# Optimization experiments

Hardware: AMD Instinct MI355X
Metric: run time of the kernel (lower is better)

Reference implementation:

```python
import jax, jax.numpy as jnp
import numpy as np

B, P, H, W, K = 2, 4096, 128, 128, 8
RADIUS = 0.05  # NDC-space point radius (raster_settings.radius)


def setup_inputs() -> dict:
    key = jax.random.key(0)
    k1, k2, k3 = jax.random.split(key, 3)
    points_world = jax.random.normal(k1, (B, P, 3), jnp.float32)
    # near-identity rotation (row-vector convention: X_view = X_world @ R + T)
    R = jnp.eye(3, dtype=jnp.float32)[None] + 0.01 * jax.random.normal(k2, (B, 3, 3), jnp.float32)
    # translate cloud to z ~ +3 so points are in front of the camera
    T = (0.1 * jax.random.normal(k3, (B, 3), jnp.float32)).at[:, 2].add(3.0)
    focal = jnp.full((B,), 1.5, jnp.float32)
    return {"points_world": points_world, "R": R, "T": T, "focal": focal}


def reference(points_world, R, T, focal):
    # --- camera transform: world -> view -> NDC (z kept in view space) ---
    pts_view = jnp.einsum('bpi,bij->bpj', points_world, R) + T[:, None, :]  # [B,P,3]
    z = pts_view[..., 2]                                                    # [B,P]
    x_ndc = focal[:, None] * pts_view[..., 0] / z
    y_ndc = focal[:, None] * pts_view[..., 1] / z

    # --- pixel-center NDC grid (pytorch3d convention: +x left, +y up) ---
    gx = 1.0 - 2.0 * (jnp.arange(W, dtype=jnp.float32) + 0.5) / W  # [W]
    gy = 1.0 - 2.0 * (jnp.arange(H, dtype=jnp.float32) + 0.5) / H  # [H]
    GY, GX = jnp.meshgrid(gy, gx, indexing='ij')
    gxf = GX.reshape(-1)  # [HW]
    gyf = GY.reshape(-1)

    # --- per-pixel candidate search: squared NDC distance to every point ---
    dist2 = (gxf[None, :, None] - x_ndc[:, None, :]) ** 2 \
          + (gyf[None, :, None] - y_ndc[:, None, :]) ** 2      # [B,HW,P]
    inside = (dist2 < RADIUS * RADIUS) & (z[:, None, :] > 0.0)  # in radius & in front

    # --- depth-sorted top-K nearest-in-z among covering points ---
    keyz = jnp.where(inside, z[:, None, :], jnp.inf)            # [B,HW,P]
    neg_top, idx_top = jax.lax.top_k(-keyz, K)                  # K smallest z
    zk = jnp.take_along_axis(keyz, idx_top, axis=-1)            # [B,HW,K]
    dk = jnp.take_along_axis(dist2, idx_top, axis=-1)
    valid = jnp.isfinite(zk)

    idx = jnp.where(valid, idx_top, -1).reshape(B, H, W, K)
    zbuf = jnp.where(valid, zk, -1.0).reshape(B, H, W, K)
    dists = jnp.where(valid, dk, -1.0).reshape(B, H, W, K)
    return idx, zbuf, dists
```

## Files before the change

### kernel.cpp

```cpp
#include <hip/hip_runtime.h>
#include <math.h>

#define BB 2
#define PP 4096
#define HH 128
#define WW 128
#define KK 8
#define TS 8
#define NTX (WW / TS)
#define NTY (HH / TS)
#define NW 4
#define SEG (PP / NW)

__global__ __launch_bounds__(64 * NW, 2) void raster_kernel(
    const float* __restrict__ pw,
    const float* __restrict__ Rm,
    const float* __restrict__ Tv,
    const float* __restrict__ fo,
    float* __restrict__ out,
    int N)
{
    __shared__ float4 cand[NW][SEG];

    const int tx = blockIdx.x, ty = blockIdx.y, b = blockIdx.z;
    const int wv   = threadIdx.x >> 6;
    const int lane = threadIdx.x & 63;

    const float* r = Rm + b * 9;
    const float r00=r[0], r01=r[1], r02=r[2];
    const float r10=r[3], r11=r[4], r12=r[5];
    const float r20=r[6], r21=r[7], r22=r[8];
    const float t0=Tv[b*3+0], t1=Tv[b*3+1], t2=Tv[b*3+2];
    const float f = fo[b];

    const float R2f   = (float)(0.05 * 0.05);
    const float apron = 0.05f + 1e-5f;

    float gx_hi = 1.0f - 2.0f * ((float)(tx * TS)          + 0.5f) / (float)WW;
    float gx_lo = 1.0f - 2.0f * ((float)(tx * TS + TS - 1) + 0.5f) / (float)WW;
    float gy_hi = 1.0f - 2.0f * ((float)(ty * TS)          + 0.5f) / (float)HH;
    float gy_lo = 1.0f - 2.0f * ((float)(ty * TS + TS - 1) + 0.5f) / (float)HH;
    const float xmin = gx_lo - apron, xmax = gx_hi + apron;
    const float ymin = gy_lo - apron, ymax = gy_hi + apron;

    int cnt = 0;
    const float* pwb = pw + (size_t)b * PP * 3;
    const float* qp = pwb + (wv * SEG + lane) * 3;
    float cx = qp[0], cy = qp[1], cz = qp[2];
    for (int it = 0; it < SEG / 64; ++it) {
        float nx = 0.f, ny = 0.f, nz = 0.f;
        if (it + 1 < SEG / 64) {
            const float* qn = qp + (it + 1) * 192;
            nx = qn[0]; ny = qn[1]; nz = qn[2];
        }
        int i = wv * SEG + it * 64 + lane;
        float x = cx, y = cy, z = cz;
        float vx = __fadd_rn(__fadd_rn(__fadd_rn(__fmul_rn(x, r00), __fmul_rn(y, r10)), __fmul_rn(z, r20)), t0);
        float vy = __fadd_rn(__fadd_rn(__fadd_rn(__fmul_rn(x, r01), __fmul_rn(y, r11)), __fmul_rn(z, r21)), t1);
        float vz = __fadd_rn(__fadd_rn(__fadd_rn(__fmul_rn(x, r02), __fmul_rn(y, r12)), __fmul_rn(z, r22)), t2);
        float xn = __fmul_rn(f, vx) / vz;
        float yn = __fmul_rn(f, vy) / vz;
        bool keep = (vz > 0.0f) && (xn >= xmin) && (xn <= xmax)
                                && (yn >= ymin) && (yn <= ymax);
        unsigned long long m = __ballot(keep);
        if (keep) {
            int pos = __popcll(m & ((1ull << lane) - 1ull));
            cand[wv][cnt + pos] = make_float4(xn, yn, vz, __int_as_float(i));
        }
        cnt += __popcll(m);
        cx = nx; cy = ny; cz = nz;
    }

    int w = tx * TS + (lane & (TS - 1));
    int h = ty * TS + (lane / TS);
    float gx = 1.0f - 2.0f * ((float)w + 0.5f) / (float)WW;
    float gy = 1.0f - 2.0f * ((float)h + 0.5f) / (float)HH;

    float zk[KK], dk[KK]; int ik[KK];
#pragma unroll
    for (int j = 0; j < KK; ++j) { zk[j] = INFINITY; dk[j] = -1.0f; ik[j] = -1; }

    auto proc = [&](float4 q) {
        float dx = __fsub_rn(gx, q.x);
        float dy = __fsub_rn(gy, q.y);
        float d2 = __fadd_rn(__fmul_rn(dx, dx), __fmul_rn(dy, dy));
        float z = q.z;
        if (d2 < R2f && z < zk[KK - 1]) {
            int i = __float_as_int(q.w);
#pragma unroll
            for (int j = KK - 1; j >= 1; --j) {
                if (z < zk[j]) {
                    if (z < zk[j - 1]) { zk[j] = zk[j-1]; ik[j] = ik[j-1]; dk[j] = dk[j-1]; }
                    else               { zk[j] = z;       ik[j] = i;       dk[j] = d2;      }
                }
            }
            if (z < zk[0]) { zk[0] = z; ik[0] = i; dk[0] = d2; }
        }
    };

    int s = 0;
    for (; s + 4 <= cnt; s += 4) {
        float4 q0 = cand[wv][s];
        float4 q1 = cand[wv][s + 1];
        float4 q2 = cand[wv][s + 2];
        float4 q3 = cand[wv][s + 3];
        proc(q0); proc(q1); proc(q2); proc(q3);
    }
    for (; s < cnt; ++s) proc(cand[wv][s]);

    __syncthreads();
    float* mz = (float*)&cand[0][0];
    float* mi = mz + NW * KK * 64;
    float* md = mi + NW * KK * 64;
#pragma unroll
    for (int sj = 0; sj < KK; ++sj) {
        mz[(wv * KK + sj) * 64 + lane] = zk[sj];
        mi[(wv * KK + sj) * 64 + lane] = __int_as_float(ik[sj]);
        md[(wv * KK + sj) * 64 + lane] = dk[sj];
    }
    __syncthreads();

    if (lane < 16) {
        const int pe = wv * 16 + lane;
        float hz[NW], hd[NW]; int hi_[NW], hp[NW];
#pragma unroll
        for (int wq = 0; wq < NW; ++wq) {
            hp[wq]  = 0;
            hz[wq]  = mz[(wq * KK) * 64 + pe];
            hi_[wq] = __float_as_int(mi[(wq * KK) * 64 + pe]);
            hd[wq]  = md[(wq * KK) * 64 + pe];
        }
        float A[KK], Z[KK], D[KK];
#pragma unroll
        for (int o = 0; o < KK; ++o) {
            int bw = 0;
#pragma unroll
            for (int wq = 1; wq < NW; ++wq) {
                bool better = (hz[wq] < hz[bw]) ||
                              ((hz[wq] == hz[bw]) && (hi_[wq] < hi_[bw]));
                if (better) bw = wq;
            }
            float sz = hz[0], sd = hd[0]; int si = hi_[0];
#pragma unroll
            for (int wq = 1; wq < NW; ++wq) {
                if (bw == wq) { sz = hz[wq]; sd = hd[wq]; si = hi_[wq]; }
            }
            A[o] = (float)si;
            Z[o] = (si >= 0) ? sz : -1.0f;
            D[o] = sd;
#pragma unroll
            for (int wq = 0; wq < NW; ++wq) {
                if (bw == wq) {
                    int p = ++hp[wq];
                    if (p < KK) {
                        hz[wq]  = mz[(wq * KK + p) * 64 + pe];
                        hi_[wq] = __float_as_int(mi[(wq * KK + p) * 64 + pe]);
                        hd[wq]  = md[(wq * KK + p) * 64 + pe];
                    } else {
                        hz[wq] = INFINITY; hi_[wq] = -1; hd[wq] = -1.0f;
                    }
                }
            }
        }
        int w2 = tx * TS + (pe & (TS - 1));
        int h2 = ty * TS + (pe / TS);
        int pix  = (b * HH + h2) * WW + w2;
        int base = pix * KK;
        float4* oa = (float4*)(out + base);
        float4* oz = (float4*)(out + N + base);
        float4* od = (float4*)(out + 2 * N + base);
        oa[0] = ((float4*)A)[0]; oa[1] = ((float4*)A)[1];
        oz[0] = ((float4*)Z)[0]; oz[1] = ((float4*)Z)[1];
        od[0] = ((float4*)D)[0]; od[1] = ((float4*)D)[1];
    }
}

extern "C" void kernel_launch(void* const* d_in, const int* in_sizes, int n_in,
                              void* d_out, int out_size, void* d_ws, size_t ws_size,
                              hipStream_t stream) {
    const float* pw = (const float*)d_in[0];
    const float* Rm = (const float*)d_in[1];
    const float* Tv = (const float*)d_in[2];
    const float* fo = (const float*)d_in[3];
    int N = out_size / 3;

    hipLaunchKernelGGL(raster_kernel, dim3(NTX, NTY, BB), dim3(64 * NW), 0, stream,
                       pw, Rm, Tv, fo, (float*)d_out, N);
}
```

Baseline: 79.80 us.

## Bin projected points into per-tile lists before per-tile top-K search

Replaces the per-tile scan of all points, in which every tile block re-projects all 4096 points, with a two-pass scheme. A binning kernel projects each point once and appends it through atomics to the lists of the tiles its radius overlaps. A top-K kernel then reads only its tile's list from global memory and splits it across four waves. Ties are now broken by index so the order stays deterministic despite atomic append order. The cost is a memset, an extra launch and global atomics, and a tile's list is silently truncated if it exceeds CAP.

After: 102.1 us. 27.9% more time.

```diff
diff --git a/kernel.cpp b/kernel.cpp
--- a/kernel.cpp
+++ b/kernel.cpp
@@ -9,16 +9,189 @@
 #define TS 8
 #define NTX (WW / TS)
 #define NTY (HH / TS)
+#define NTILES (NTX * NTY)
 #define NW 4
 #define SEG (PP / NW)
-
-__global__ __launch_bounds__(64 * NW, 2) void raster_kernel(
+#define CAP 2048
+#define LIST_OFF 4096
+#define WS_NEEDED ((size_t)LIST_OFF + (size_t)BB * NTILES * CAP * sizeof(float4))
+
+
+__global__ __launch_bounds__(256, 4) void bin_kernel(
     const float* __restrict__ pw,
     const float* __restrict__ Rm,
     const float* __restrict__ Tv,
     const float* __restrict__ fo,
+    int* __restrict__ cnt,
+    float4* __restrict__ lst)
+{
+    int gid = blockIdx.x * 256 + threadIdx.x;
+    if (gid >= BB * PP) return;
+    int b = gid >> 12;
+    int p = gid & (PP - 1);
+
+    const float* r = Rm + b * 9;
+    const float r00=r[0], r01=r[1], r02=r[2];
+    const float r10=r[3], r11=r[4], r12=r[5];
+    const float r20=r[6], r21=r[7], r22=r[8];
+    const float t0=Tv[b*3+0], t1=Tv[b*3+1], t2=Tv[b*3+2];
+    const float f = fo[b];
+
+    const float* q = pw + (size_t)gid * 3;
+    float x = q[0], y = q[1], z = q[2];
+    float vx = __fadd_rn(__fadd_rn(__fadd_rn(__fmul_rn(x, r00), __fmul_rn(y, r10)), __fmul_rn(z, r20)), t0);
+    float vy = __fadd_rn(__fadd_rn(__fadd_rn(__fmul_rn(x, r01), __fmul_rn(y, r11)), __fmul_rn(z, r21)), t1);
+    float vz = __fadd_rn(__fadd_rn(__fadd_rn(__fmul_rn(x, r02), __fmul_rn(y, r12)), __fmul_rn(z, r22)), t2);
+    if (!(vz > 0.0f)) return;
+    float xn = __fmul_rn(f, vx) / vz;
+    float yn = __fmul_rn(f, vy) / vz;
+    if (!(xn > -1.06f && xn < 1.06f && yn > -1.06f && yn < 1.06f)) return;
+
+    const float axs = (float)WW * 0.0502f;
+    float Ax = (float)WW * (1.0f - xn);
+    float Ay = (float)HH * (1.0f - yn);
+    int txlo = (int)ceilf ((Ax - axs - (float)(2 * TS - 1)) * (1.0f / (2 * TS)));
+    int txhi = (int)floorf((Ax + axs - 1.0f)                * (1.0f / (2 * TS)));
+    int tylo = (int)ceilf ((Ay - axs - (float)(2 * TS - 1)) * (1.0f / (2 * TS)));
+    int tyhi = (int)floorf((Ay + axs - 1.0f)                * (1.0f / (2 * TS)));
+    txlo = max(txlo, 0); txhi = min(txhi, NTX - 1);
+    tylo = max(tylo, 0); tyhi = min(tyhi, NTY - 1);
+
+    float4 rec = make_float4(xn, yn, vz, __int_as_float(p));
+    for (int ty = tylo; ty <= tyhi; ++ty)
+        for (int tx = txlo; tx <= txhi; ++tx) {
+            int t = (b * NTY + ty) * NTX + tx;
+            int slot = atomicAdd(&cnt[t], 1);
+            if (slot < CAP) lst[(size_t)t * CAP + slot] = rec;
+        }
+}
+
+__global__ __launch_bounds__(64 * NW, 2) void topk_kernel(
+    const int* __restrict__ cnt,
+    const float4* __restrict__ lst,
     float* __restrict__ out,
     int N)
+{
+    __shared__ float mbuf[3 * NW * KK * 64];
+
+    const int tx = blockIdx.x, ty = blockIdx.y, b = blockIdx.z;
+    const int wv   = threadIdx.x >> 6;
+    const int lane = threadIdx.x & 63;
+    const int t = (b * NTY + ty) * NTX + tx;
+
+    int c = cnt[t]; c = (c > CAP) ? CAP : c;
+    const float4* q = lst + (size_t)t * CAP;
+
+    int w = tx * TS + (lane & (TS - 1));
+    int h = ty * TS + (lane / TS);
+    float gx = 1.0f - 2.0f * ((float)w + 0.5f) / (float)WW;
+    float gy = 1.0f - 2.0f * ((float)h + 0.5f) / (float)HH;
+
+    const float R2f = (float)(0.05 * 0.05);
+    float zk[KK], dk[KK]; int ik[KK];
+#pragma unroll
+    for (int j = 0; j < KK; ++j) { zk[j] = INFINITY; dk[j] = -1.0f; ik[j] = -1; }
+
+    auto proc = [&](float4 qq) {
+        float dx = __fsub_rn(gx, qq.x);
+        float dy = __fsub_rn(gy, qq.y);
+        float d2 = __fadd_rn(__fmul_rn(dx, dx), __fmul_rn(dy, dy));
+        float z = qq.z;
+        int   i = __float_as_int(qq.w);
+        bool lt_last = (z < zk[KK-1]) || ((z == zk[KK-1]) && (i < ik[KK-1]));
+        if (d2 < R2f && lt_last) {
+#pragma unroll
+            for (int j = KK - 1; j >= 1; --j) {
+                bool ltj  = (z < zk[j])   || ((z == zk[j])   && (i < ik[j]));
+                bool ltjm = (z < zk[j-1]) || ((z == zk[j-1]) && (i < ik[j-1]));
+                if (ltj) {
+                    if (ltjm) { zk[j] = zk[j-1]; ik[j] = ik[j-1]; dk[j] = dk[j-1]; }
+                    else      { zk[j] = z;       ik[j] = i;       dk[j] = d2;      }
+                }
+            }
+            bool lt0 = (z < zk[0]) || ((z == zk[0]) && (i < ik[0]));
+            if (lt0) { zk[0] = z; ik[0] = i; dk[0] = d2; }
+        }
+    };
+
+    int c0 = (c * wv) / NW, c1 = (c * (wv + 1)) / NW;
+    int s = c0;
+    for (; s + 4 <= c1; s += 4) {
+        float4 q0 = q[s], q1 = q[s + 1], q2 = q[s + 2], q3 = q[s + 3];
+        proc(q0); proc(q1); proc(q2); proc(q3);
+    }
+    for (; s < c1; ++s) proc(q[s]);
+
+    float* mz = mbuf;
+    float* mi = mz + NW * KK * 64;
+    float* md = mi + NW * KK * 64;
+#pragma unroll
+    for (int sj = 0; sj < KK; ++sj) {
+        mz[(wv * KK + sj) * 64 + lane] = zk[sj];
+        mi[(wv * KK + sj) * 64 + lane] = __int_as_float(ik[sj]);
+        md[(wv * KK + sj) * 64 + lane] = dk[sj];
+    }
+    __syncthreads();
+
+    if (lane < 16) {
+        const int pe = wv * 16 + lane;
+        float hz[NW], hd[NW]; int hi_[NW], hp[NW];
+#pragma unroll
+        for (int wq = 0; wq < NW; ++wq) {
+            hp[wq]  = 0;
+            hz[wq]  = mz[(wq * KK) * 64 + pe];
+            hi_[wq] = __float_as_int(mi[(wq * KK) * 64 + pe]);
+            hd[wq]  = md[(wq * KK) * 64 + pe];
+        }
+        float A[KK], Z[KK], D[KK];
+#pragma unroll
+        for (int o = 0; o < KK; ++o) {
+            int bw = 0;
+#pragma unroll
+            for (int wq = 1; wq < NW; ++wq) {
+                bool better = (hz[wq] < hz[bw]) ||
+                              ((hz[wq] == hz[bw]) && (hi_[wq] < hi_[bw]));
+                if (better) bw = wq;
+            }
+            float sz = hz[0], sd = hd[0]; int si = hi_[0];
+#pragma unroll
+            for (int wq = 1; wq < NW; ++wq) {
+                if (bw == wq) { sz = hz[wq]; sd = hd[wq]; si = hi_[wq]; }
+            }
+            A[o] = (float)si;
+            Z[o] = (si >= 0) ? sz : -1.0f;
+            D[o] = sd;
+#pragma unroll
+            for (int wq = 0; wq < NW; ++wq) {
+                if (bw == wq) {
+                    int pp2 = ++hp[wq];
+                    if (pp2 < KK) {
+                        hz[wq]  = mz[(wq * KK + pp2) * 64 + pe];
+                        hi_[wq] = __float_as_int(mi[(wq * KK + pp2) * 64 + pe]);
+                        hd[wq]  = md[(wq * KK + pp2) * 64 + pe];
+                    } else {
+                        hz[wq] = INFINITY; hi_[wq] = -1; hd[wq] = -1.0f;
+                    }
+                }
+            }
+        }
+        int w2 = tx * TS + (pe & (TS - 1));
+        int h2 = ty * TS + (pe / TS);
+        int pix  = (b * HH + h2) * WW + w2;
+        int base = pix * KK;
+        float4* oa = (float4*)(out + base);
+        float4* oz = (float4*)(out + N + base);
+        float4* od = (float4*)(out + 2 * N + base);
+        oa[0] = ((float4*)A)[0]; oa[1] = ((float4*)A)[1];
+        oz[0] = ((float4*)Z)[0]; oz[1] = ((float4*)Z)[1];
+        od[0] = ((float4*)D)[0]; od[1] = ((float4*)D)[1];
+    }
+}
+
+__global__ __launch_bounds__(64 * NW, 2) void raster_fallback(
+    const float* __restrict__ pw, const float* __restrict__ Rm,
+    const float* __restrict__ Tv, const float* __restrict__ fo,
+    float* __restrict__ out, int N)
 {
     __shared__ float4 cand[NW][SEG];
 
@@ -184,6 +357,16 @@
     const float* fo = (const float*)d_in[3];
     int N = out_size / 3;
 
-    hipLaunchKernelGGL(raster_kernel, dim3(NTX, NTY, BB), dim3(64 * NW), 0, stream,
-                       pw, Rm, Tv, fo, (float*)d_out, N);
+    if (d_ws != nullptr && ws_size >= WS_NEEDED) {
+        int*    cnt = (int*)d_ws;
+        float4* lst = (float4*)((char*)d_ws + LIST_OFF);
+        hipMemsetAsync(d_ws, 0, (size_t)BB * NTILES * sizeof(int), stream);
+        hipLaunchKernelGGL(bin_kernel, dim3((BB * PP + 255) / 256), dim3(256), 0, stream,
+                           pw, Rm, Tv, fo, cnt, lst);
+        hipLaunchKernelGGL(topk_kernel, dim3(NTX, NTY, BB), dim3(64 * NW), 0, stream,
+                           cnt, lst, (float*)d_out, N);
+    } else {
+        hipLaunchKernelGGL(raster_fallback, dim3(NTX, NTY, BB), dim3(64 * NW), 0, stream,
+                           pw, Rm, Tv, fo, (float*)d_out, N);
+    }
 }
```
